# Optimization experiments

Hardware: AMD Instinct MI355X
Metric: run time of the kernel (lower is better)

The kernel has to match this reference:

```python
import jax, jax.numpy as jnp
import numpy as np

TWO_PI = 2.0 * np.pi
D_IN, N, P, C, BATCH = 784, 1024, 128, 10, 256
T, BETA, K_COUP, A_ANC = 0.5, 2.0, 1.0, 0.08
OMEGA_ANC = TWO_PI * 200.0
N_STEPS = 16  # fixed-grid RK4 steps over [0, T]


def setup_inputs() -> dict:
    key = jax.random.key(0)
    k0, k1, k2, k3 = jax.random.split(key, 4)
    x = jax.random.normal(k0, (BATCH, D_IN), dtype=jnp.float32)
    W_enc = jax.random.normal(k1, (N, D_IN), dtype=jnp.float32) * (1.0 / np.sqrt(D_IN))
    b_enc = jnp.zeros((N,), dtype=jnp.float32)
    xi = jax.random.uniform(k2, (P, N), dtype=jnp.float32) * TWO_PI  # memory patterns
    W_out = jax.random.normal(k3, (C, 2 * N), dtype=jnp.float32) * (1.0 / np.sqrt(2 * N))
    b_out = jnp.zeros((C,), dtype=jnp.float32)
    return {"x": x, "W_enc": W_enc, "b_enc": b_enc, "xi": xi, "W_out": W_out, "b_out": b_out}


def _dphi(t, phi, xi):
    # phi: (B, N), xi: (P, N) -> diff: (B, P, N)
    diff = phi[:, None, :] - xi[None, :, :]
    m = jnp.cos(diff).sum(-1)                               # (B, P) overlaps
    w = jax.nn.softmax(BETA * m / N, axis=-1)               # (B, P)
    coupling = jnp.einsum('bp,bpn->bn', w, jnp.sin(diff))   # (B, N)
    return K_COUP * coupling + A_ANC * jnp.sin(OMEGA_ANC * t - phi)


def reference(x, W_enc, b_enc, xi, W_out, b_out):
    # Encoder: phi0 in (0, 2pi)
    phi0 = TWO_PI * jax.nn.sigmoid(x @ W_enc.T + b_enc)
    dt = T / N_STEPS

    def step(phi, t):
        k1 = _dphi(t, phi, xi)
        k2 = _dphi(t + 0.5 * dt, phi + 0.5 * dt * k1, xi)
        k3 = _dphi(t + 0.5 * dt, phi + 0.5 * dt * k2, xi)
        k4 = _dphi(t + dt, phi + dt * k3, xi)
        return phi + (dt / 6.0) * (k1 + 2.0 * k2 + 2.0 * k3 + k4), None

    ts = jnp.arange(N_STEPS, dtype=jnp.float32) * dt
    phi_T, _ = jax.lax.scan(step, phi0, ts)
    # Readout on [cos, sin] features
    feats = jnp.concatenate([jnp.cos(phi_T), jnp.sin(phi_T)], axis=-1)
    return feats @ W_out.T + b_out
```

## Files before the change

kernel.cpp:

```cpp
#include <hip/hip_runtime.h>
#include <math.h>


typedef __attribute__((ext_vector_type(4))) float f32x4;
typedef __attribute__((ext_vector_type(4))) int   i32x4;
typedef __attribute__((ext_vector_type(8))) short bf16x8;

struct TCons { float s[64]; float c[64]; };

__device__ __forceinline__ unsigned short f2bf(float f) {
  unsigned u = __builtin_bit_cast(unsigned, f);
  return (unsigned short)((u + 0x7FFFu + ((u >> 16) & 1u)) >> 16);
}
__device__ __forceinline__ int pk4i8(const float* v) {
  int a = __float2int_rn(v[0]*127.0f) & 255;
  int b = __float2int_rn(v[1]*127.0f) & 255;
  int c = __float2int_rn(v[2]*127.0f) & 255;
  int d = __float2int_rn(v[3]*127.0f);
  return a | (b << 8) | (c << 16) | (d << 24);
}

#define A1_OFF    0
#define MBUF_OFF  4096
#define W_OFF     5152
#define ZP_OFF    5408
#define XST_OFF   5424
#define T2L_OFF   7104
#define RED_OFF   7104
#define LDS_BYTES 154560

__global__
__attribute__((amdgpu_flat_work_group_size(1024, 1024), amdgpu_waves_per_eu(4, 4)))
void phasenn_kernel(
    const float* __restrict__ x, const float* __restrict__ W_enc,
    const float* __restrict__ b_enc, const float* __restrict__ xi,
    const float* __restrict__ W_out, const float* __restrict__ b_out,
    float* __restrict__ dout, char* __restrict__ wsb, TCons tc)
{
  __shared__ __align__(16) char smem[LDS_BYTES];

  const int tid  = threadIdx.x;
  const int bk   = blockIdx.x;
  const int w    = tid >> 6;
  const int lane = tid & 63;
  const int q    = lane >> 4;
  const int b16  = lane & 15;
  const int j4   = b16 >> 2;
  const int r4   = b16 & 3;
  const int nph  = (w*4 + j4)*16 + q*4 + r4;

  char* T1g = wsb;
  char* T2g = wsb + (256 << 10);

  if (tid < 4) *(unsigned*)(smem + ZP_OFF + tid*4) = 0;

  if (tid < 100) {
    const int dg = tid;
    bf16x8 fr = {0,0,0,0,0,0,0,0};
    if (dg < 98) {
      f32x4 v0 = *(const f32x4*)(x + (size_t)bk*784 + dg*8);
      f32x4 v1 = *(const f32x4*)(x + (size_t)bk*784 + dg*8 + 4);
      #pragma unroll
      for (int i = 0; i < 8; ++i) fr[i] = (short)f2bf(i < 4 ? v0[i] : v1[i-4]);
    }
    *(bf16x8*)(smem + XST_OFF + (dg << 4)) = fr;
  }

  if (w < 8) {
    const int p = w*16 + b16;
    for (int F = 0; F < 16; ++F) {
      const int n0 = F*64 + q*16;
      f32x4 v0 = *(const f32x4*)(xi + p*1024 + n0);
      f32x4 v1 = *(const f32x4*)(xi + p*1024 + n0 + 4);
      f32x4 v2 = *(const f32x4*)(xi + p*1024 + n0 + 8);
      f32x4 v3 = *(const f32x4*)(xi + p*1024 + n0 + 12);
      int cu[16], su[16];
      #pragma unroll
      for (int i = 0; i < 16; ++i) {
        float xv = (i < 4) ? v0[i] : (i < 8) ? v1[i-4] : (i < 12) ? v2[i-8] : v3[i-12];
        su[i] = __float2int_rn(__sinf(xv)*7.0f) + 8;
        cu[i] = __float2int_rn(__cosf(xv)*7.0f) + 8;
      }
      unsigned pc0=0, pc1=0, ps0=0, ps1=0;
      #pragma unroll
      for (int i = 0; i < 4; ++i) {
        pc0 |= (unsigned)(cu[i]     | (cu[i+4]  << 4)) << (8*i);
        pc1 |= (unsigned)(cu[8+i]   | (cu[12+i] << 4)) << (8*i);
        ps0 |= (unsigned)(su[i]     | (su[i+4]  << 4)) << (8*i);
        ps1 |= (unsigned)(su[8+i]   | (su[12+i] << 4)) << (8*i);
      }
      i32x4 P = {(int)pc0, (int)pc1, (int)ps0, (int)ps1};
      *(i32x4*)(T1g + (size_t)(w*16 + F)*1024 + lane*16) = P;
    }
  } else {
    const int w2 = w - 8;
    for (int f = 0; f < 16; ++f) {
      const int ct = w2*8 + (f >> 1), P2 = f & 1;
      const int n = ct*16 + b16;
      float cv[16], sv[16];
      #pragma unroll
      for (int i = 0; i < 16; ++i) {
        float xv = xi[(P2*64 + q*16 + i)*1024 + n];
        sv[i] = __sinf(xv); cv[i] = __cosf(xv);
      }
      i32x4 C = { pk4i8(cv), pk4i8(cv+4), pk4i8(cv+8), pk4i8(cv+12) };
      i32x4 S = { pk4i8(sv), pk4i8(sv+4), pk4i8(sv+8), pk4i8(sv+12) };
      char* dst = (ct < 36)
          ? (smem + T2L_OFF + (size_t)(ct*2 + P2)*2048 + lane*16)
          : (T2g + (size_t)(ct*2 + P2)*2048 + lane*16);
      *(i32x4*)(dst) = C; *(i32x4*)(dst + 1024) = S;
    }
  }
  __syncthreads();

  float p0, ka, pwv;
  {
    f32x4 pac[4] = {{0,0,0,0},{0,0,0,0},{0,0,0,0},{0,0,0,0}};
    for (int kt = 0; kt < 25; ++kt) {
      bf16x8 bfr = *(const bf16x8*)(smem + XST_OFF + ((kt*4 + q) << 4));
      const int d = kt*32 + q*8;
      #pragma unroll
      for (int j = 0; j < 4; ++j) {
        bf16x8 afr = {0,0,0,0,0,0,0,0};
        if (d < 784) {
          const int n = (w*4 + j)*16 + b16;
          f32x4 v0 = *(const f32x4*)(W_enc + n*784 + d);
          f32x4 v1 = *(const f32x4*)(W_enc + n*784 + d + 4);
          #pragma unroll
          for (int i = 0; i < 8; ++i) afr[i] = (short)f2bf(i < 4 ? v0[i] : v1[i-4]);
        }
        pac[j] = __builtin_amdgcn_mfma_f32_16x16x32_bf16(afr, bfr, pac[j], 0, 0, 0);
      }
    }
    f32x4 pc = (j4==0) ? pac[0] : (j4==1) ? pac[1] : (j4==2) ? pac[2] : pac[3];
    float vA = (r4==0) ? pc[0] : (r4==1) ? pc[1] : (r4==2) ? pc[2] : pc[3];
    float ph = 6.283185307179586f / (1.0f + __expf(-(vA + b_enc[nph])));
    p0 = ph; pwv = ph; ka = 0.0f;
  }

  const float dtf = 0.03125f, half = 0.015625f;
  const float sixth = (float)(0.03125/6.0);
  const float mscale = (float)(2.0 / (1024.0 * 889.0));
  const float kscale = (float)(1.0 / 16129.0);

  char* a1wr = smem + A1_OFF + nph;

  for (int e = 0; e < 64; ++e) {
    float csv, snv;
    {
      snv = __sinf(pwv);
      csv = __cosf(pwv);
      *(char*)(a1wr)        = (char)(__float2int_rn(csv*127.0f));
      *(char*)(a1wr + 1024) = (char)(__float2int_rn(snv*127.0f));
    }
    __syncthreads();

    {
      const int pt = w & 7, kh = w >> 3;
      i32x4 accC = {0,0,0,0}, accS = {0,0,0,0};
      const char* t1b = T1g + (size_t)(pt*16 + kh*8)*1024 + lane*16;
      const char* a1b = smem + A1_OFF + kh*512 + q*16;
      const unsigned M = 0x0F0F0F0Fu;
      #pragma unroll
      for (int i2 = 0; i2 < 8; ++i2) {
        i32x4 pk = *(const i32x4*)(t1b + (size_t)i2*1024);
        i32x4 ca = { (int)((unsigned)pk[0] & M), (int)(((unsigned)pk[0] >> 4) & M),
                     (int)((unsigned)pk[1] & M), (int)(((unsigned)pk[1] >> 4) & M) };
        i32x4 sa = { (int)((unsigned)pk[2] & M), (int)(((unsigned)pk[2] >> 4) & M),
                     (int)((unsigned)pk[3] & M), (int)(((unsigned)pk[3] >> 4) & M) };
        i32x4 bc = *(const i32x4*)(a1b + i2*64);
        i32x4 bs = *(const i32x4*)(a1b + i2*64 + 1024);
        accC = __builtin_amdgcn_mfma_i32_16x16x64_i8(ca, bc, accC, 0, 0, 0);
        accS = __builtin_amdgcn_mfma_i32_16x16x64_i8(sa, bs, accS, 0, 0, 0);
      }
      if (b16 == 0) {
        i32x4 acc = accC + accS;
        *(i32x4*)(smem + MBUF_OFF + kh*528 + ((pt*16 + q*4) << 2)) = acc;
      }
    }
    __syncthreads();

    if (w == 0) {
      const char* mb = smem + MBUF_OFF + lane*8;
      int a0 = *(const int*)(mb),       a1 = *(const int*)(mb + 4);
      int b0 = *(const int*)(mb + 528), b1 = *(const int*)(mb + 528 + 4);
      float e0 = __expf((float)(a0 + b0) * mscale);
      float e1 = __expf((float)(a1 + b1) * mscale);
      float s = e0 + e1;
      #pragma unroll
      for (int off = 1; off < 64; off <<= 1) s += __shfl_xor(s, off, 64);
      const float inv = 127.0f / s;
      int w0 = __float2int_rn(e0 * inv);
      int w1 = __float2int_rn(e1 * inv);
      *(unsigned short*)(smem + W_OFF + lane*2) =
          (unsigned short)((w0 & 255) | (w1 << 8));
    }
    __syncthreads();

    {
      const float swt = tc.s[e], cwt = tc.c[e];
      const int st = e & 3;
      i32x4 wf0 = *(const i32x4*)(smem + W_OFF + q*16);
      i32x4 wf1 = *(const i32x4*)(smem + W_OFF + 64 + q*16);
      i32x4 aC[4] = {{0,0,0,0},{0,0,0,0},{0,0,0,0},{0,0,0,0}};
      i32x4 aS[4] = {{0,0,0,0},{0,0,0,0},{0,0,0,0},{0,0,0,0}};
      if (w < 9) {
        const char* t2b = smem + T2L_OFF + (size_t)(w*8)*2048 + lane*16;
        #pragma unroll
        for (int c = 0; c < 4; ++c)
          #pragma unroll
          for (int P2 = 0; P2 < 2; ++P2) {
            i32x4 ct_ = *(const i32x4*)(t2b + (size_t)(c*2 + P2)*2048);
            i32x4 st_ = *(const i32x4*)(t2b + (size_t)(c*2 + P2)*2048 + 1024);
            i32x4 wf = P2 ? wf1 : wf0;
            aC[c] = __builtin_amdgcn_mfma_i32_16x16x64_i8(ct_, wf, aC[c], 0, 0, 0);
            aS[c] = __builtin_amdgcn_mfma_i32_16x16x64_i8(st_, wf, aS[c], 0, 0, 0);
          }
      } else {
        const char* t2b = T2g + (size_t)(w*8)*2048 + lane*16;
        #pragma unroll
        for (int c = 0; c < 4; ++c)
          #pragma unroll
          for (int P2 = 0; P2 < 2; ++P2) {
            i32x4 ct_ = *(const i32x4*)(t2b + (size_t)(c*2 + P2)*2048);
            i32x4 st_ = *(const i32x4*)(t2b + (size_t)(c*2 + P2)*2048 + 1024);
            i32x4 wf = P2 ? wf1 : wf0;
            aC[c] = __builtin_amdgcn_mfma_i32_16x16x64_i8(ct_, wf, aC[c], 0, 0, 0);
            aS[c] = __builtin_amdgcn_mfma_i32_16x16x64_i8(st_, wf, aS[c], 0, 0, 0);
          }
      }
      i32x4 c4 = (j4==0) ? aC[0] : (j4==1) ? aC[1] : (j4==2) ? aC[2] : aC[3];
      i32x4 s4 = (j4==0) ? aS[0] : (j4==1) ? aS[1] : (j4==2) ? aS[2] : aS[3];
      float vC = (float)((r4==0) ? c4[0] : (r4==1) ? c4[1] : (r4==2) ? c4[2] : c4[3]);
      float vS = (float)((r4==0) ? s4[0] : (r4==1) ? s4[1] : (r4==2) ? s4[2] : s4[3]);
      float kv = (snv*vC - csv*vS) * kscale
               + 0.08f*(swt*csv - cwt*snv);
      if (st == 0)      { ka  = kv;           pwv = p0 + kv*half; }
      else if (st == 1) { ka += 2.0f*kv;      pwv = p0 + kv*half; }
      else if (st == 2) { ka += 2.0f*kv;      pwv = p0 + kv*dtf;  }
      else { ka += kv; p0 += ka*sixth; pwv = p0; }
    }
  }

  __syncthreads();
  {
    *(unsigned short*)(smem + A1_OFF + nph*2)        = f2bf(__cosf(p0));
    *(unsigned short*)(smem + A1_OFF + 2048 + nph*2) = f2bf(__sinf(p0));
  }
  __syncthreads();
  {
    f32x4 acc = {0.f, 0.f, 0.f, 0.f};
    #pragma unroll
    for (int i2 = 0; i2 < 4; ++i2) {
      const int kt = w*4 + i2;
      const int k = kt*32 + q*8;
      bf16x8 afr = {0,0,0,0,0,0,0,0};
      if (b16 < 10) {
        f32x4 v0 = *(const f32x4*)(W_out + b16*2048 + k);
        f32x4 v1 = *(const f32x4*)(W_out + b16*2048 + k + 4);
        #pragma unroll
        for (int i = 0; i < 8; ++i) afr[i] = (short)f2bf(i < 4 ? v0[i] : v1[i-4]);
      }
      const char* baddr = (b16 == 0)
          ? (smem + A1_OFF + ((kt*4 + q) << 4))
          : (smem + ZP_OFF);
      bf16x8 bfr = *(const bf16x8*)baddr;
      acc = __builtin_amdgcn_mfma_f32_16x16x32_bf16(afr, bfr, acc, 0, 0, 0);
    }
    *(f32x4*)(smem + RED_OFF + ((w*64 + lane) << 4)) = acc;
  }
  __syncthreads();
  if (tid < 64) {
    f32x4 s = {0.f, 0.f, 0.f, 0.f};
    #pragma unroll
    for (int w2 = 0; w2 < 16; ++w2)
      s += *(const f32x4*)(smem + RED_OFF + ((w2*64 + tid) << 4));
    const int b = tid & 15, q2 = tid >> 4;
    if (b == 0) {
      #pragma unroll
      for (int r = 0; r < 4; ++r) {
        const int cl = q2*4 + r;
        if (cl < 10)
          dout[(size_t)bk*10 + cl] = s[r] + b_out[cl];
      }
    }
  }
}

extern "C" void kernel_launch(void* const* d_in, const int* in_sizes, int n_in,
                              void* d_out, int out_size, void* d_ws, size_t ws_size,
                              hipStream_t stream) {
  (void)in_sizes; (void)n_in; (void)ws_size; (void)out_size;
  const float* x     = (const float*)d_in[0];
  const float* W_enc = (const float*)d_in[1];
  const float* b_enc = (const float*)d_in[2];
  const float* xi    = (const float*)d_in[3];
  const float* W_out = (const float*)d_in[4];
  const float* b_out = (const float*)d_in[5];
  float* out = (float*)d_out;
  char* wsb = (char*)d_ws;

  TCons tc;
  const double OME = 2.0 * 3.14159265358979323846 * 200.0;
  const double dtd = 0.03125;
  const double co[4] = {0.0, 0.5, 0.5, 1.0};
  for (int e = 0; e < 64; ++e) {
    double t = ((double)(e >> 2) + co[e & 3]) * dtd;
    tc.s[e] = (float)sin(OME * t);
    tc.c[e] = (float)cos(OME * t);
  }

  phasenn_kernel<<<dim3(256), dim3(1024), 0, stream>>>(
      x, W_enc, b_enc, xi, W_out, b_out, out, wsb, tc);
}
```

Measured before the change: 348.0 us.

## Pack second-stage xi cos/sin tables as 4-bit nibbles, all in LDS

The per-step coupling table (cos/sin of xi) is quantized to offset 4-bit values packed two per byte instead of int8. This halves its size so it fits entirely in LDS, which removes the global-memory path previously used by the waves whose tiles did not fit. Nibbles are unpacked with masks into int8 lanes for the MFMA, and the +8 offset is corrected by subtracting 8 times the sum of the quantized softmax weights, computed with an extra wave reduction. It trades coarser numerical precision and extra ALU unpacking for fewer global loads in the hot loop.

```diff
diff --git a/kernel.cpp b/kernel.cpp
--- a/kernel.cpp
+++ b/kernel.cpp
@@ -11,13 +11,6 @@
 __device__ __forceinline__ unsigned short f2bf(float f) {
   unsigned u = __builtin_bit_cast(unsigned, f);
   return (unsigned short)((u + 0x7FFFu + ((u >> 16) & 1u)) >> 16);
-}
-__device__ __forceinline__ int pk4i8(const float* v) {
-  int a = __float2int_rn(v[0]*127.0f) & 255;
-  int b = __float2int_rn(v[1]*127.0f) & 255;
-  int c = __float2int_rn(v[2]*127.0f) & 255;
-  int d = __float2int_rn(v[3]*127.0f);
-  return a | (b << 8) | (c << 16) | (d << 24);
 }
 
 #define A1_OFF    0
@@ -27,7 +20,7 @@
 #define XST_OFF   5424
 #define T2L_OFF   7104
 #define RED_OFF   7104
-#define LDS_BYTES 154560
+#define LDS_BYTES 138176
 
 __global__
 __attribute__((amdgpu_flat_work_group_size(1024, 1024), amdgpu_waves_per_eu(4, 4)))
@@ -50,7 +43,6 @@
   const int nph  = (w*4 + j4)*16 + q*4 + r4;
 
   char* T1g = wsb;
-  char* T2g = wsb + (256 << 10);
 
   if (tid < 4) *(unsigned*)(smem + ZP_OFF + tid*4) = 0;
 
@@ -97,18 +89,23 @@
     for (int f = 0; f < 16; ++f) {
       const int ct = w2*8 + (f >> 1), P2 = f & 1;
       const int n = ct*16 + b16;
-      float cv[16], sv[16];
+      int cu[16], su[16];
       #pragma unroll
       for (int i = 0; i < 16; ++i) {
         float xv = xi[(P2*64 + q*16 + i)*1024 + n];
-        sv[i] = __sinf(xv); cv[i] = __cosf(xv);
-      }
-      i32x4 C = { pk4i8(cv), pk4i8(cv+4), pk4i8(cv+8), pk4i8(cv+12) };
-      i32x4 S = { pk4i8(sv), pk4i8(sv+4), pk4i8(sv+8), pk4i8(sv+12) };
-      char* dst = (ct < 36)
-          ? (smem + T2L_OFF + (size_t)(ct*2 + P2)*2048 + lane*16)
-          : (T2g + (size_t)(ct*2 + P2)*2048 + lane*16);
-      *(i32x4*)(dst) = C; *(i32x4*)(dst + 1024) = S;
+        su[i] = __float2int_rn(__sinf(xv)*7.0f) + 8;
+        cu[i] = __float2int_rn(__cosf(xv)*7.0f) + 8;
+      }
+      unsigned pc0=0, pc1=0, ps0=0, ps1=0;
+      #pragma unroll
+      for (int i = 0; i < 4; ++i) {
+        pc0 |= (unsigned)(cu[i]     | (cu[i+4]  << 4)) << (8*i);
+        pc1 |= (unsigned)(cu[8+i]   | (cu[12+i] << 4)) << (8*i);
+        ps0 |= (unsigned)(su[i]     | (su[i+4]  << 4)) << (8*i);
+        ps1 |= (unsigned)(su[8+i]   | (su[12+i] << 4)) << (8*i);
+      }
+      i32x4 P = {(int)pc0, (int)pc1, (int)ps0, (int)ps1};
+      *(i32x4*)(smem + T2L_OFF + (size_t)(ct*2 + P2)*1024 + lane*16) = P;
     }
   }
   __syncthreads();
@@ -141,7 +138,7 @@
   const float dtf = 0.03125f, half = 0.015625f;
   const float sixth = (float)(0.03125/6.0);
   const float mscale = (float)(2.0 / (1024.0 * 889.0));
-  const float kscale = (float)(1.0 / 16129.0);
+  const float kscale = (float)(1.0 / 889.0);
 
   char* a1wr = smem + A1_OFF + nph;
 
@@ -194,6 +191,10 @@
       int w1 = __float2int_rn(e1 * inv);
       *(unsigned short*)(smem + W_OFF + lane*2) =
           (unsigned short)((w0 & 255) | (w1 << 8));
+      int sw = w0 + w1;
+      #pragma unroll
+      for (int off = 1; off < 64; off <<= 1) sw += __shfl_xor(sw, off, 64);
+      if (lane == 0) *(int*)(smem + W_OFF + 128) = sw;
     }
     __syncthreads();
 
@@ -202,37 +203,30 @@
       const int st = e & 3;
       i32x4 wf0 = *(const i32x4*)(smem + W_OFF + q*16);
       i32x4 wf1 = *(const i32x4*)(smem + W_OFF + 64 + q*16);
+      const int bias8 = 8 * (*(const int*)(smem + W_OFF + 128));
       i32x4 aC[4] = {{0,0,0,0},{0,0,0,0},{0,0,0,0},{0,0,0,0}};
       i32x4 aS[4] = {{0,0,0,0},{0,0,0,0},{0,0,0,0},{0,0,0,0}};
-      if (w < 9) {
-        const char* t2b = smem + T2L_OFF + (size_t)(w*8)*2048 + lane*16;
+      const char* t2b = smem + T2L_OFF + (size_t)(w*8)*1024 + lane*16;
+      const unsigned M = 0x0F0F0F0Fu;
+      #pragma unroll
+      for (int c = 0; c < 4; ++c)
         #pragma unroll
-        for (int c = 0; c < 4; ++c)
-          #pragma unroll
-          for (int P2 = 0; P2 < 2; ++P2) {
-            i32x4 ct_ = *(const i32x4*)(t2b + (size_t)(c*2 + P2)*2048);
-            i32x4 st_ = *(const i32x4*)(t2b + (size_t)(c*2 + P2)*2048 + 1024);
-            i32x4 wf = P2 ? wf1 : wf0;
-            aC[c] = __builtin_amdgcn_mfma_i32_16x16x64_i8(ct_, wf, aC[c], 0, 0, 0);
-            aS[c] = __builtin_amdgcn_mfma_i32_16x16x64_i8(st_, wf, aS[c], 0, 0, 0);
-          }
-      } else {
-        const char* t2b = T2g + (size_t)(w*8)*2048 + lane*16;
-        #pragma unroll
-        for (int c = 0; c < 4; ++c)
-          #pragma unroll
-          for (int P2 = 0; P2 < 2; ++P2) {
-            i32x4 ct_ = *(const i32x4*)(t2b + (size_t)(c*2 + P2)*2048);
-            i32x4 st_ = *(const i32x4*)(t2b + (size_t)(c*2 + P2)*2048 + 1024);
-            i32x4 wf = P2 ? wf1 : wf0;
-            aC[c] = __builtin_amdgcn_mfma_i32_16x16x64_i8(ct_, wf, aC[c], 0, 0, 0);
-            aS[c] = __builtin_amdgcn_mfma_i32_16x16x64_i8(st_, wf, aS[c], 0, 0, 0);
-          }
-      }
+        for (int P2 = 0; P2 < 2; ++P2) {
+          i32x4 pk = *(const i32x4*)(t2b + (size_t)(c*2 + P2)*1024);
+          i32x4 ct_ = { (int)((unsigned)pk[0] & M), (int)(((unsigned)pk[0] >> 4) & M),
+                        (int)((unsigned)pk[1] & M), (int)(((unsigned)pk[1] >> 4) & M) };
+          i32x4 st_ = { (int)((unsigned)pk[2] & M), (int)(((unsigned)pk[2] >> 4) & M),
+                        (int)((unsigned)pk[3] & M), (int)(((unsigned)pk[3] >> 4) & M) };
+          i32x4 wf = P2 ? wf1 : wf0;
+          aC[c] = __builtin_amdgcn_mfma_i32_16x16x64_i8(ct_, wf, aC[c], 0, 0, 0);
+          aS[c] = __builtin_amdgcn_mfma_i32_16x16x64_i8(st_, wf, aS[c], 0, 0, 0);
+        }
       i32x4 c4 = (j4==0) ? aC[0] : (j4==1) ? aC[1] : (j4==2) ? aC[2] : aC[3];
       i32x4 s4 = (j4==0) ? aS[0] : (j4==1) ? aS[1] : (j4==2) ? aS[2] : aS[3];
-      float vC = (float)((r4==0) ? c4[0] : (r4==1) ? c4[1] : (r4==2) ? c4[2] : c4[3]);
-      float vS = (float)((r4==0) ? s4[0] : (r4==1) ? s4[1] : (r4==2) ? s4[2] : s4[3]);
+      int iC = (r4==0) ? c4[0] : (r4==1) ? c4[1] : (r4==2) ? c4[2] : c4[3];
+      int iS = (r4==0) ? s4[0] : (r4==1) ? s4[1] : (r4==2) ? s4[2] : s4[3];
+      float vC = (float)(iC - bias8);
+      float vS = (float)(iS - bias8);
       float kv = (snv*vC - csv*vS) * kscale
                + 0.08f*(swt*csv - cwt*snv);
       if (st == 0)      { ka  = kv;           pwv = p0 + kv*half; }
```

Result: slower. 358.5 us (+3.0%).
